# Performance work log

Measured on AMD Instinct MI355X. Metric: run time of the kernel, lower is better.

Reference implementation:

```python
import jax, jax.numpy as jnp
import numpy as np

VOCAB = 128000
H = 256
L = 65536  # complete binary tree: 2**16 leaves -> 16 merge levels


def setup_inputs() -> dict:
    key = jax.random.key(0)
    ks = jax.random.split(key, 10)
    tokens = jax.random.randint(ks[0], (L,), 0, VOCAB)
    emb = jax.random.normal(ks[1], (VOCAB, H), dtype=jnp.float32) * 0.05
    # 5 gate projections per side (r_l, r_r, z_l, z_r, z), torch Linear layout (out, in)
    WL = jax.random.normal(ks[2], (5, H, H), dtype=jnp.float32) * 0.05
    WR = jax.random.normal(ks[3], (5, H, H), dtype=jnp.float32) * 0.05
    bL = jax.random.normal(ks[4], (5, H), dtype=jnp.float32) * 0.05
    bR = jax.random.normal(ks[5], (5, H), dtype=jnp.float32) * 0.05
    # candidate projections self.l / self.r
    Wlh = jax.random.normal(ks[6], (H, H), dtype=jnp.float32) * 0.05
    Wrh = jax.random.normal(ks[7], (H, H), dtype=jnp.float32) * 0.05
    blh = jax.random.normal(ks[8], (H,), dtype=jnp.float32) * 0.05
    brh = jax.random.normal(ks[9], (H,), dtype=jnp.float32) * 0.05
    return {"tokens": tokens, "emb": emb, "WL": WL, "WR": WR, "bL": bL,
            "bR": bR, "Wlh": Wlh, "Wrh": Wrh, "blh": blh, "brh": brh}


def reference(tokens, emb, WL, WR, bL, bR, Wlh, Wrh, blh, brh):
    cur = emb[tokens]  # [L, H] leaf states (embedding lookup)
    n_levels = int(np.log2(cur.shape[0]))
    bias = (bL + bR)[:, None, :]  # [5, 1, H]
    for _ in range(n_levels):
        left = cur[0::2]   # [N, H]
        right = cur[1::2]  # [N, H]
        # all 5 sigmoid gates in one batched contraction (torch Linear: x @ W.T + b)
        pre = (jnp.einsum('nh,goh->gno', left, WL)
               + jnp.einsum('nh,goh->gno', right, WR) + bias)  # [5, N, H]
        g = jax.nn.sigmoid(pre)
        r_l, r_r, z_l, z_r, z = g[0], g[1], g[2], g[3], g[4]
        h_tilde = jnp.tanh((r_l * left) @ Wlh.T + (r_r * right) @ Wrh.T + blh + brh)
        cur = z_l * left + z_r * right + z * h_tilde
    h = cur[0]  # [H] root state
    return (h, h, h)
```

## Files before the change

kernel.cpp:

```cpp
#include <hip/hip_runtime.h>
#include <hip/hip_bf16.h>
#include <string.h>

#define H 256
#define K2 512
#define BM 64
#define THREADS 512
#define LTOT 65536

typedef __attribute__((ext_vector_type(8))) short short8;
typedef __attribute__((ext_vector_type(4))) float f32x4;

struct __align__(8) S4 { short x, y, z, w; };

__device__ __forceinline__ short f2bf(float f) {
    union { float f; unsigned u; } v; v.f = f;
    unsigned r = v.u + 0x7fffu + ((v.u >> 16) & 1u);
    return (short)(r >> 16);
}
__device__ __forceinline__ float bf2f(short s) {
    union { unsigned u; float f; } v; v.u = ((unsigned)(unsigned short)s) << 16;
    return v.f;
}
__device__ __forceinline__ float sigm(float x) {
    return 1.f / (1.f + __expf(-x));
}
__device__ __forceinline__ int swz(int row, int kbytes) {
    return ((row << 10) + kbytes) ^ ((row & 7) << 4);
}

__global__ void prep_kernel(const float* __restrict__ WL, const float* __restrict__ WR,
                            const float* __restrict__ Wlh, const float* __restrict__ Wrh,
                            const float* __restrict__ bL, const float* __restrict__ bR,
                            const float* __restrict__ blh, const float* __restrict__ brh,
                            short* __restrict__ W1, short* __restrict__ W2,
                            float* __restrict__ pb, float* __restrict__ hb) {
    int i = blockIdx.x * blockDim.x + threadIdx.x;
    const int nW1 = 5 * H * K2;
    if (i < nW1) {
        int g = i / (H * K2);
        int rem = i % (H * K2);
        int o = rem / K2, k = rem % K2;
        float v = (k < H) ? WL[(g * H + o) * H + k] : WR[(g * H + o) * H + (k - H)];
        W1[i] = f2bf(v);
        return;
    }
    int j = i - nW1;
    if (j < H * K2) {
        int o = j / K2, k = j % K2;
        float v = (k < H) ? Wlh[o * H + k] : Wrh[o * H + (k - H)];
        W2[j] = f2bf(v);
        return;
    }
    int p = j - H * K2;
    if (p < 5 * H) { pb[p] = bL[p] + bR[p]; return; }
    int q = p - 5 * H;
    if (q < H) { hb[q] = blh[q] + brh[q]; }
}

__device__ __forceinline__ void gemm_pass(const short* Abuf, const short* __restrict__ Wg,
                                          int colbase, int l15, int khalf, f32x4 acc[4][2]) {
#pragma unroll
    for (int mt = 0; mt < 4; ++mt) {
        acc[mt][0] = (f32x4){0.f, 0.f, 0.f, 0.f};
        acc[mt][1] = (f32x4){0.f, 0.f, 0.f, 0.f};
    }
#pragma unroll
    for (int kk = 0; kk < 16; ++kk) {
        int kel = kk * 32 + khalf * 8;
        int kb = kel * 2;
        short8 b0 = *(const short8*)(Wg + (colbase + l15) * K2 + kel);
        short8 b1 = *(const short8*)(Wg + (colbase + 16 + l15) * K2 + kel);
#pragma unroll
        for (int mt = 0; mt < 4; ++mt) {
            int row = mt * 16 + l15;
            short8 a = *(const short8*)((const char*)Abuf + swz(row, kb));
            acc[mt][0] = __builtin_amdgcn_mfma_f32_16x16x32_bf16(a, b0, acc[mt][0], 0, 0, 0);
            acc[mt][1] = __builtin_amdgcn_mfma_f32_16x16x32_bf16(a, b1, acc[mt][1], 0, 0, 0);
        }
    }
}

__global__ __launch_bounds__(THREADS, 2) void level_kernel(
    const float* __restrict__ curIn, const int* __restrict__ tokens,
    const float* __restrict__ emb, float* __restrict__ curOut,
    const short* __restrict__ W1, const short* __restrict__ W2,
    const float* __restrict__ pb, const float* __restrict__ hb, int N) {
    __shared__ __align__(16) short A1[BM * K2];
    __shared__ __align__(16) short A2[BM * K2];
    const int tid = threadIdx.x;
    const int n0 = blockIdx.x * BM;

#pragma unroll
    for (int it = 0; it < 16; ++it) {
        int c = tid + it * THREADS;
        int f = c * 4;
        int r = f >> 8;
        int col = f & 255;
        int gr = 2 * n0 + r;
        float4 v = make_float4(0.f, 0.f, 0.f, 0.f);
        if (gr < 2 * N) {
            const float* src = tokens ? (emb + (size_t)tokens[gr] * H) : (curIn + (size_t)gr * H);
            v = *(const float4*)(src + col);
        }
        int row = r >> 1;
        int k = ((r & 1) << 8) | col;
        S4 s; s.x = f2bf(v.x); s.y = f2bf(v.y); s.z = f2bf(v.z); s.w = f2bf(v.w);
        *(S4*)((char*)A1 + swz(row, k * 2)) = s;
    }
    __syncthreads();

    const int wave = tid >> 6, lane = tid & 63;
    const int l15 = lane & 15, khalf = lane >> 4;
    const int colbase = wave * 32;

    f32x4 acc[4][2];

#pragma unroll
    for (int g = 0; g < 2; ++g) {
        gemm_pass(A1, W1 + g * H * K2, colbase, l15, khalf, acc);
#pragma unroll
        for (int nt = 0; nt < 2; ++nt) {
            int col = colbase + nt * 16 + l15;
            float bias = pb[g * H + col];
            int koff2 = (((g << 8) | col)) * 2;
#pragma unroll
            for (int mt = 0; mt < 4; ++mt) {
#pragma unroll
                for (int j = 0; j < 4; ++j) {
                    int row = mt * 16 + khalf * 4 + j;
                    float rg = sigm(acc[mt][nt][j] + bias);
                    float xv = bf2f(*(const short*)((const char*)A1 + swz(row, koff2)));
                    *(short*)((char*)A2 + swz(row, koff2)) = f2bf(rg * xv);
                }
            }
        }
    }
    __syncthreads();

    float ht[4][2][4];
    gemm_pass(A2, W2, colbase, l15, khalf, acc);
#pragma unroll
    for (int nt = 0; nt < 2; ++nt) {
        int col = colbase + nt * 16 + l15;
        float bias = hb[col];
#pragma unroll
        for (int mt = 0; mt < 4; ++mt)
#pragma unroll
            for (int j = 0; j < 4; ++j)
                ht[mt][nt][j] = tanhf(acc[mt][nt][j] + bias);
    }

    float outv[4][2][4];
#pragma unroll
    for (int g = 2; g < 4; ++g) {
        gemm_pass(A1, W1 + g * H * K2, colbase, l15, khalf, acc);
#pragma unroll
        for (int nt = 0; nt < 2; ++nt) {
            int col = colbase + nt * 16 + l15;
            float bias = pb[g * H + col];
#pragma unroll
            for (int mt = 0; mt < 4; ++mt)
#pragma unroll
                for (int j = 0; j < 4; ++j) {
                    int rl = mt * 16 + khalf * 4 + j;
                    int gr = n0 + rl;
                    float z = sigm(acc[mt][nt][j] + bias);
                    float v = 0.f;
                    if (gr < N) {
                        int srow = 2 * gr + (g - 2);
                        v = tokens ? emb[(size_t)tokens[srow] * H + col]
                                   : curIn[(size_t)srow * H + col];
                    }
                    if (g == 2) outv[mt][nt][j] = z * v;
                    else        outv[mt][nt][j] += z * v;
                }
        }
    }

    gemm_pass(A1, W1 + 4 * H * K2, colbase, l15, khalf, acc);
#pragma unroll
    for (int nt = 0; nt < 2; ++nt) {
        int col = colbase + nt * 16 + l15;
        float bias = pb[4 * H + col];
#pragma unroll
        for (int mt = 0; mt < 4; ++mt)
#pragma unroll
            for (int j = 0; j < 4; ++j) {
                int rl = mt * 16 + khalf * 4 + j;
                int gr = n0 + rl;
                float z = sigm(acc[mt][nt][j] + bias);
                float o = outv[mt][nt][j] + z * ht[mt][nt][j];
                if (gr < N) curOut[(size_t)gr * H + col] = o;
            }
    }
}

__global__ void finalize_kernel(const float* __restrict__ h, float* __restrict__ out) {
    int i = threadIdx.x;
    if (i < 768) out[i] = h[i & 255];
}

extern "C" void kernel_launch(void* const* d_in, const int* in_sizes, int n_in,
                              void* d_out, int out_size, void* d_ws, size_t ws_size,
                              hipStream_t stream) {
    const int*   tokens = (const int*)d_in[0];
    const float* emb    = (const float*)d_in[1];
    const float* WL     = (const float*)d_in[2];
    const float* WR     = (const float*)d_in[3];
    const float* bL     = (const float*)d_in[4];
    const float* bR     = (const float*)d_in[5];
    const float* Wlh    = (const float*)d_in[6];
    const float* Wrh    = (const float*)d_in[7];
    const float* blh    = (const float*)d_in[8];
    const float* brh    = (const float*)d_in[9];

    char* ws = (char*)d_ws;
    short* W1 = (short*)ws;
    short* W2 = W1 + 5 * H * K2;
    float* pb = (float*)(W2 + H * K2);
    float* hb = pb + 5 * H;
    float* bufB = (float*)(ws + 2 * 1024 * 1024);
    float* bufA = bufB + (size_t)32768 * H;

    {
        int total = 5 * H * K2 + H * K2 + 5 * H + H;
        int blocks = (total + 255) / 256;
        prep_kernel<<<blocks, 256, 0, stream>>>(WL, WR, Wlh, Wrh, bL, bR, blh, brh,
                                                W1, W2, pb, hb);
    }

    const float* in = nullptr;
    for (int l = 0; l < 16; ++l) {
        int N = 32768 >> l;
        float* out = (l & 1) ? bufA : bufB;
        int blocks = (N + BM - 1) / BM;
        level_kernel<<<blocks, THREADS, 0, stream>>>(
            in, (l == 0) ? tokens : nullptr, emb, out, W1, W2, pb, hb, N);
        in = out;
    }

    finalize_kernel<<<1, 768, 0, stream>>>(bufA, (float*)d_out);
}
```

Baseline: 1.497 ms.

## Fuse gate GEMMs per pass and collapse small tail levels into one block

Restructures the level kernel so the two reset gates share one K-loop and the three update gates share another, reusing each A fragment across several weight matrices instead of re-reading it per gate. The final combine now reads the children from the bf16 LDS tile rather than reloading them from global memory. Levels 9-15, which each have at most one block of work, are folded into a single persistent tail kernel, which also writes the output and removes seven launches plus the finalize kernel. A fast exp-based tanh replaces tanhf. The costs are higher register pressure from the larger accumulator arrays and reduced precision, since the gated sum now uses bf16-rounded children.

```diff
diff --git a/kernel.cpp b/kernel.cpp
--- a/kernel.cpp
+++ b/kernel.cpp
@@ -1,12 +1,11 @@
 #include <hip/hip_runtime.h>
 #include <hip/hip_bf16.h>
-#include <string.h>
 
 #define H 256
 #define K2 512
 #define BM 64
 #define THREADS 512
-#define LTOT 65536
+#define HK2 (H * K2)
 
 typedef __attribute__((ext_vector_type(8))) short short8;
 typedef __attribute__((ext_vector_type(4))) float f32x4;
@@ -24,6 +23,10 @@
 }
 __device__ __forceinline__ float sigm(float x) {
     return 1.f / (1.f + __expf(-x));
+}
+__device__ __forceinline__ float tanh_f(float x) {
+    float e = __expf(2.f * x);
+    return 1.f - 2.f / (e + 1.f);
 }
 __device__ __forceinline__ int swz(int row, int kbytes) {
     return ((row << 10) + kbytes) ^ ((row & 7) << 4);
@@ -36,48 +39,221 @@
                             short* __restrict__ W1, short* __restrict__ W2,
                             float* __restrict__ pb, float* __restrict__ hb) {
     int i = blockIdx.x * blockDim.x + threadIdx.x;
-    const int nW1 = 5 * H * K2;
+    const int nW1 = 5 * HK2;
     if (i < nW1) {
-        int g = i / (H * K2);
-        int rem = i % (H * K2);
+        int g = i / HK2;
+        int rem = i % HK2;
         int o = rem / K2, k = rem % K2;
         float v = (k < H) ? WL[(g * H + o) * H + k] : WR[(g * H + o) * H + (k - H)];
         W1[i] = f2bf(v);
         return;
     }
     int j = i - nW1;
-    if (j < H * K2) {
+    if (j < HK2) {
         int o = j / K2, k = j % K2;
         float v = (k < H) ? Wlh[o * H + k] : Wrh[o * H + (k - H)];
         W2[j] = f2bf(v);
         return;
     }
-    int p = j - H * K2;
+    int p = j - HK2;
     if (p < 5 * H) { pb[p] = bL[p] + bR[p]; return; }
     int q = p - 5 * H;
     if (q < H) { hb[q] = blh[q] + brh[q]; }
 }
 
-__device__ __forceinline__ void gemm_pass(const short* Abuf, const short* __restrict__ Wg,
-                                          int colbase, int l15, int khalf, f32x4 acc[4][2]) {
-#pragma unroll
-    for (int mt = 0; mt < 4; ++mt) {
-        acc[mt][0] = (f32x4){0.f, 0.f, 0.f, 0.f};
-        acc[mt][1] = (f32x4){0.f, 0.f, 0.f, 0.f};
-    }
+__device__ __forceinline__ void do_level(const float* __restrict__ curIn,
+                                         const int* __restrict__ tokens,
+                                         const float* __restrict__ emb,
+                                         float* __restrict__ curOut,
+                                         const short* __restrict__ W1,
+                                         const short* __restrict__ W2,
+                                         const float* __restrict__ pb,
+                                         const float* __restrict__ hb,
+                                         int N, int n0, short* A1, short* A2) {
+    const int tid = threadIdx.x;
+    __syncthreads();
+
+#pragma unroll
+    for (int it = 0; it < 16; ++it) {
+        int c = tid + it * THREADS;
+        int r = c >> 6;
+        int col = (c & 63) << 2;
+        int gr = 2 * n0 + r;
+        float4 v = make_float4(0.f, 0.f, 0.f, 0.f);
+        if (gr < 2 * N) {
+            const float* src = tokens ? (emb + (size_t)tokens[gr] * H)
+                                      : (curIn + (size_t)gr * H);
+            v = *(const float4*)(src + col);
+        }
+        int row = r >> 1;
+        int kel = ((r & 1) << 8) | col;
+        S4 s; s.x = f2bf(v.x); s.y = f2bf(v.y); s.z = f2bf(v.z); s.w = f2bf(v.w);
+        *(S4*)((char*)A1 + swz(row, kel * 2)) = s;
+    }
+    __syncthreads();
+
+    const int wave = tid >> 6, lane = tid & 63;
+    const int l15 = lane & 15, khalf = lane >> 4;
+    const int col0 = wave * 32;
+
+    f32x4 acc1[2][4][2];
+#pragma unroll
+    for (int g = 0; g < 2; ++g)
+#pragma unroll
+        for (int rt = 0; rt < 4; ++rt)
+#pragma unroll
+            for (int ct = 0; ct < 2; ++ct)
+                acc1[g][rt][ct] = (f32x4){0.f, 0.f, 0.f, 0.f};
+
+    const short* b1p[2][2];
+#pragma unroll
+    for (int g = 0; g < 2; ++g)
+#pragma unroll
+        for (int ct = 0; ct < 2; ++ct)
+            b1p[g][ct] = W1 + g * HK2 + (size_t)(col0 + ct * 16 + l15) * K2 + khalf * 8;
+
 #pragma unroll
     for (int kk = 0; kk < 16; ++kk) {
-        int kel = kk * 32 + khalf * 8;
-        int kb = kel * 2;
-        short8 b0 = *(const short8*)(Wg + (colbase + l15) * K2 + kel);
-        short8 b1 = *(const short8*)(Wg + (colbase + 16 + l15) * K2 + kel);
-#pragma unroll
-        for (int mt = 0; mt < 4; ++mt) {
-            int row = mt * 16 + l15;
-            short8 a = *(const short8*)((const char*)Abuf + swz(row, kb));
-            acc[mt][0] = __builtin_amdgcn_mfma_f32_16x16x32_bf16(a, b0, acc[mt][0], 0, 0, 0);
-            acc[mt][1] = __builtin_amdgcn_mfma_f32_16x16x32_bf16(a, b1, acc[mt][1], 0, 0, 0);
+        short8 a[4];
+#pragma unroll
+        for (int rt = 0; rt < 4; ++rt)
+            a[rt] = *(const short8*)((const char*)A1 + swz(rt * 16 + l15, kk * 64 + khalf * 16));
+        short8 b[2][2];
+#pragma unroll
+        for (int g = 0; g < 2; ++g)
+#pragma unroll
+            for (int ct = 0; ct < 2; ++ct)
+                b[g][ct] = *(const short8*)(b1p[g][ct] + kk * 32);
+#pragma unroll
+        for (int g = 0; g < 2; ++g)
+#pragma unroll
+            for (int rt = 0; rt < 4; ++rt)
+#pragma unroll
+                for (int ct = 0; ct < 2; ++ct)
+                    acc1[g][rt][ct] = __builtin_amdgcn_mfma_f32_16x16x32_bf16(
+                        a[rt], b[g][ct], acc1[g][rt][ct], 0, 0, 0);
+    }
+
+#pragma unroll
+    for (int g = 0; g < 2; ++g)
+#pragma unroll
+        for (int ct = 0; ct < 2; ++ct) {
+            int col = col0 + ct * 16 + l15;
+            float bias = pb[g * H + col];
+            int koff2 = ((g << 8) | col) * 2;
+#pragma unroll
+            for (int rt = 0; rt < 4; ++rt)
+#pragma unroll
+                for (int j = 0; j < 4; ++j) {
+                    int row = rt * 16 + khalf * 4 + j;
+                    float rg = sigm(acc1[g][rt][ct][j] + bias);
+                    float xv = bf2f(*(const short*)((const char*)A1 + swz(row, koff2)));
+                    *(short*)((char*)A2 + swz(row, koff2)) = f2bf(rg * xv);
+                }
         }
+    __syncthreads();
+
+    f32x4 acc2[4][2];
+#pragma unroll
+    for (int rt = 0; rt < 4; ++rt)
+#pragma unroll
+        for (int ct = 0; ct < 2; ++ct)
+            acc2[rt][ct] = (f32x4){0.f, 0.f, 0.f, 0.f};
+
+    const short* b2p[2];
+#pragma unroll
+    for (int ct = 0; ct < 2; ++ct)
+        b2p[ct] = W2 + (size_t)(col0 + ct * 16 + l15) * K2 + khalf * 8;
+
+#pragma unroll
+    for (int kk = 0; kk < 16; ++kk) {
+        short8 a[4];
+#pragma unroll
+        for (int rt = 0; rt < 4; ++rt)
+            a[rt] = *(const short8*)((const char*)A2 + swz(rt * 16 + l15, kk * 64 + khalf * 16));
+        short8 b[2];
+#pragma unroll
+        for (int ct = 0; ct < 2; ++ct)
+            b[ct] = *(const short8*)(b2p[ct] + kk * 32);
+#pragma unroll
+        for (int rt = 0; rt < 4; ++rt)
+#pragma unroll
+            for (int ct = 0; ct < 2; ++ct)
+                acc2[rt][ct] = __builtin_amdgcn_mfma_f32_16x16x32_bf16(
+                    a[rt], b[ct], acc2[rt][ct], 0, 0, 0);
+    }
+
+    float ht[4][2][4];
+#pragma unroll
+    for (int ct = 0; ct < 2; ++ct) {
+        int col = col0 + ct * 16 + l15;
+        float bias = hb[col];
+#pragma unroll
+        for (int rt = 0; rt < 4; ++rt)
+#pragma unroll
+            for (int j = 0; j < 4; ++j)
+                ht[rt][ct][j] = tanh_f(acc2[rt][ct][j] + bias);
+    }
+
+    f32x4 acc3[3][4][2];
+#pragma unroll
+    for (int g = 0; g < 3; ++g)
+#pragma unroll
+        for (int rt = 0; rt < 4; ++rt)
+#pragma unroll
+            for (int ct = 0; ct < 2; ++ct)
+                acc3[g][rt][ct] = (f32x4){0.f, 0.f, 0.f, 0.f};
+
+    const short* b3p[3][2];
+#pragma unroll
+    for (int g = 0; g < 3; ++g)
+#pragma unroll
+        for (int ct = 0; ct < 2; ++ct)
+            b3p[g][ct] = W1 + (g + 2) * HK2 + (size_t)(col0 + ct * 16 + l15) * K2 + khalf * 8;
+
+#pragma unroll
+    for (int kk = 0; kk < 16; ++kk) {
+        short8 a[4];
+#pragma unroll
+        for (int rt = 0; rt < 4; ++rt)
+            a[rt] = *(const short8*)((const char*)A1 + swz(rt * 16 + l15, kk * 64 + khalf * 16));
+        short8 b[3][2];
+#pragma unroll
+        for (int g = 0; g < 3; ++g)
+#pragma unroll
+            for (int ct = 0; ct < 2; ++ct)
+                b[g][ct] = *(const short8*)(b3p[g][ct] + kk * 32);
+#pragma unroll
+        for (int g = 0; g < 3; ++g)
+#pragma unroll
+            for (int rt = 0; rt < 4; ++rt)
+#pragma unroll
+                for (int ct = 0; ct < 2; ++ct)
+                    acc3[g][rt][ct] = __builtin_amdgcn_mfma_f32_16x16x32_bf16(
+                        a[rt], b[g][ct], acc3[g][rt][ct], 0, 0, 0);
+    }
+
+#pragma unroll
+    for (int ct = 0; ct < 2; ++ct) {
+        int col = col0 + ct * 16 + l15;
+        float bzl = pb[2 * H + col];
+        float bzr = pb[3 * H + col];
+        float bzz = pb[4 * H + col];
+#pragma unroll
+        for (int rt = 0; rt < 4; ++rt)
+#pragma unroll
+            for (int j = 0; j < 4; ++j) {
+                int row = rt * 16 + khalf * 4 + j;
+                int gr = n0 + row;
+                if (gr < N) {
+                    float zl = sigm(acc3[0][rt][ct][j] + bzl);
+                    float zr = sigm(acc3[1][rt][ct][j] + bzr);
+                    float zz = sigm(acc3[2][rt][ct][j] + bzz);
+                    float xl = bf2f(*(const short*)((const char*)A1 + swz(row, col * 2)));
+                    float xr = bf2f(*(const short*)((const char*)A1 + swz(row, (col + 256) * 2)));
+                    curOut[(size_t)gr * H + col] = zl * xl + zr * xr + zz * ht[rt][ct][j];
+                }
+            }
     }
 }
 
@@ -88,117 +264,26 @@
     const float* __restrict__ pb, const float* __restrict__ hb, int N) {
     __shared__ __align__(16) short A1[BM * K2];
     __shared__ __align__(16) short A2[BM * K2];
-    const int tid = threadIdx.x;
-    const int n0 = blockIdx.x * BM;
-
-#pragma unroll
-    for (int it = 0; it < 16; ++it) {
-        int c = tid + it * THREADS;
-        int f = c * 4;
-        int r = f >> 8;
-        int col = f & 255;
-        int gr = 2 * n0 + r;
-        float4 v = make_float4(0.f, 0.f, 0.f, 0.f);
-        if (gr < 2 * N) {
-            const float* src = tokens ? (emb + (size_t)tokens[gr] * H) : (curIn + (size_t)gr * H);
-            v = *(const float4*)(src + col);
-        }
-        int row = r >> 1;
-        int k = ((r & 1) << 8) | col;
-        S4 s; s.x = f2bf(v.x); s.y = f2bf(v.y); s.z = f2bf(v.z); s.w = f2bf(v.w);
-        *(S4*)((char*)A1 + swz(row, k * 2)) = s;
+    do_level(curIn, tokens, emb, curOut, W1, W2, pb, hb, N, blockIdx.x * BM, A1, A2);
+}
+
+__global__ __launch_bounds__(THREADS, 2) void tail_kernel(
+    float* bufA, float* bufB,
+    const short* __restrict__ W1, const short* __restrict__ W2,
+    const float* __restrict__ pb, const float* __restrict__ hb,
+    float* __restrict__ out) {
+    __shared__ __align__(16) short A1[BM * K2];
+    __shared__ __align__(16) short A2[BM * K2];
+    for (int l = 9; l <= 15; ++l) {
+        int N = 32768 >> l;
+        const float* in = (l & 1) ? bufB : bufA;
+        float* o = (l & 1) ? bufA : bufB;
+        do_level(in, nullptr, nullptr, o, W1, W2, pb, hb, N, 0, A1, A2);
+        __threadfence_block();
     }
     __syncthreads();
-
-    const int wave = tid >> 6, lane = tid & 63;
-    const int l15 = lane & 15, khalf = lane >> 4;
-    const int colbase = wave * 32;
-
-    f32x4 acc[4][2];
-
-#pragma unroll
-    for (int g = 0; g < 2; ++g) {
-        gemm_pass(A1, W1 + g * H * K2, colbase, l15, khalf, acc);
-#pragma unroll
-        for (int nt = 0; nt < 2; ++nt) {
-            int col = colbase + nt * 16 + l15;
-            float bias = pb[g * H + col];
-            int koff2 = (((g << 8) | col)) * 2;
-#pragma unroll
-            for (int mt = 0; mt < 4; ++mt) {
-#pragma unroll
-                for (int j = 0; j < 4; ++j) {
-                    int row = mt * 16 + khalf * 4 + j;
-                    float rg = sigm(acc[mt][nt][j] + bias);
-                    float xv = bf2f(*(const short*)((const char*)A1 + swz(row, koff2)));
-                    *(short*)((char*)A2 + swz(row, koff2)) = f2bf(rg * xv);
-                }
-            }
-        }
-    }
-    __syncthreads();
-
-    float ht[4][2][4];
-    gemm_pass(A2, W2, colbase, l15, khalf, acc);
-#pragma unroll
-    for (int nt = 0; nt < 2; ++nt) {
-        int col = colbase + nt * 16 + l15;
-        float bias = hb[col];
-#pragma unroll
-        for (int mt = 0; mt < 4; ++mt)
-#pragma unroll
-            for (int j = 0; j < 4; ++j)
-                ht[mt][nt][j] = tanhf(acc[mt][nt][j] + bias);
-    }
-
-    float outv[4][2][4];
-#pragma unroll
-    for (int g = 2; g < 4; ++g) {
-        gemm_pass(A1, W1 + g * H * K2, colbase, l15, khalf, acc);
-#pragma unroll
-        for (int nt = 0; nt < 2; ++nt) {
-            int col = colbase + nt * 16 + l15;
-            float bias = pb[g * H + col];
-#pragma unroll
-            for (int mt = 0; mt < 4; ++mt)
-#pragma unroll
-                for (int j = 0; j < 4; ++j) {
-                    int rl = mt * 16 + khalf * 4 + j;
-                    int gr = n0 + rl;
-                    float z = sigm(acc[mt][nt][j] + bias);
-                    float v = 0.f;
-                    if (gr < N) {
-                        int srow = 2 * gr + (g - 2);
-                        v = tokens ? emb[(size_t)tokens[srow] * H + col]
-                                   : curIn[(size_t)srow * H + col];
-                    }
-                    if (g == 2) outv[mt][nt][j] = z * v;
-                    else        outv[mt][nt][j] += z * v;
-                }
-        }
-    }
-
-    gemm_pass(A1, W1 + 4 * H * K2, colbase, l15, khalf, acc);
-#pragma unroll
-    for (int nt = 0; nt < 2; ++nt) {
-        int col = colbase + nt * 16 + l15;
-        float bias = pb[4 * H + col];
-#pragma unroll
-        for (int mt = 0; mt < 4; ++mt)
-#pragma unroll
-            for (int j = 0; j < 4; ++j) {
-                int rl = mt * 16 + khalf * 4 + j;
-                int gr = n0 + rl;
-                float z = sigm(acc[mt][nt][j] + bias);
-                float o = outv[mt][nt][j] + z * ht[mt][nt][j];
-                if (gr < N) curOut[(size_t)gr * H + col] = o;
-            }
-    }
-}
-
-__global__ void finalize_kernel(const float* __restrict__ h, float* __restrict__ out) {
-    int i = threadIdx.x;
-    if (i < 768) out[i] = h[i & 255];
+    for (int i = threadIdx.x; i < 768; i += THREADS)
+        out[i] = bufA[i & 255];
 }
 
 extern "C" void kernel_launch(void* const* d_in, const int* in_sizes, int n_in,
@@ -217,21 +302,21 @@
 
     char* ws = (char*)d_ws;
     short* W1 = (short*)ws;
-    short* W2 = W1 + 5 * H * K2;
-    float* pb = (float*)(W2 + H * K2);
+    short* W2 = W1 + 5 * HK2;
+    float* pb = (float*)(W2 + HK2);
     float* hb = pb + 5 * H;
     float* bufB = (float*)(ws + 2 * 1024 * 1024);
     float* bufA = bufB + (size_t)32768 * H;
 
     {
-        int total = 5 * H * K2 + H * K2 + 5 * H + H;
+        int total = 5 * HK2 + HK2 + 5 * H + H;
         int blocks = (total + 255) / 256;
         prep_kernel<<<blocks, 256, 0, stream>>>(WL, WR, Wlh, Wrh, bL, bR, blh, brh,
                                                 W1, W2, pb, hb);
     }
 
     const float* in = nullptr;
-    for (int l = 0; l < 16; ++l) {
+    for (int l = 0; l <= 8; ++l) {
         int N = 32768 >> l;
         float* out = (l & 1) ? bufA : bufB;
         int blocks = (N + BM - 1) / BM;
@@ -240,5 +325,5 @@
         in = out;
     }
 
-    finalize_kernel<<<1, 768, 0, stream>>>(bufA, (float*)d_out);
-}
+    tail_kernel<<<1, THREADS, 0, stream>>>(bufA, bufB, W1, W2, pb, hb, (float*)d_out);
+}
```

Measured after the change: 1.436 ms. 1.04x faster.
